# Performance work log

Measured on AMD Instinct MI355X. Metric: run time of the kernel, lower is better.

## Reference

```python
import jax, jax.numpy as jnp
import numpy as np

B, M, D = 8, 8192, 1024   # batch, tokens, latent_dim
N, P = 128, 1             # num_experts, slots_per_expert
F = 4096                  # expert_dim


def setup_inputs() -> dict:
    key = jax.random.key(0)
    k_x, k_phi, k_w1, k_b1, k_w2, k_b2 = jax.random.split(key, 6)
    x = jax.random.normal(k_x, (B, M, D), dtype=jnp.float32)
    # phi initialized as randn(d, n, p) / sqrt(d) in the original
    phi = jax.random.normal(k_phi, (D, N, P), dtype=jnp.float32) / (D ** 0.5)
    # Single shared expert MLP (original aliases one nn.Sequential across all experts)
    W1 = jax.random.normal(k_w1, (D, F), dtype=jnp.float32) / (D ** 0.5)
    b1 = jax.random.normal(k_b1, (F,), dtype=jnp.float32) * 0.01
    W2 = jax.random.normal(k_w2, (F, D), dtype=jnp.float32) / (F ** 0.5)
    b2 = jax.random.normal(k_b2, (D,), dtype=jnp.float32) * 0.01
    return {"x": x, "phi": phi, "W1": W1, "b1": b1, "W2": W2, "b2": b2}


def reference(x, phi, W1, b1, W2, b2):
    # dispatch / combine logits: [b, m, n, p]
    logits = jnp.einsum('bmd,dnp->bmnp', x, phi)
    d = jax.nn.softmax(logits, axis=1)                      # softmax over tokens m
    b_, m_, n_, p_ = logits.shape
    c = jax.nn.softmax(logits.reshape(b_, m_, n_ * p_), axis=-1).reshape(b_, m_, n_, p_)
    # slot inputs: [b, n, p, d]
    x_i = jnp.einsum('bmd,bmnp->bnpd', x, d)
    # shared expert MLP (torch GELU default = exact erf)
    h = jax.nn.gelu(jnp.einsum('bnpd,df->bnpf', x_i, W1) + b1, approximate=False)
    y_i = jnp.einsum('bnpf,fd->bnpd', h, W2) + b2
    # combine: [b, m, d]
    y = jnp.einsum('bnpd,bmnp->bmd', y_i, c)
    return y
```

## Files before the change

### kernel.cpp

```cpp
#include <hip/hip_runtime.h>
#include <math.h>

#define Bq 8
#define Mq 8192
#define Dq 1024
#define Nq 128
#define Fq 4096

typedef __bf16 bf16x8 __attribute__((ext_vector_type(8)));
typedef float f32x4 __attribute__((ext_vector_type(4)));
union P4 { __bf16 h[4]; unsigned long long u; };
union H4 { short4 v; _Float16 h[4]; };
union B8 { int4 v; __bf16 h[8]; };

__device__ __forceinline__ int swz128(int row, int bcol) {
  return row * 128 + (bcol ^ ((((row & 7) ^ ((row >> 3) & 7))) << 4));
}
__device__ __forceinline__ int swz256(int row, int bcol) {
  return row * 256 + (bcol ^ ((row & 7) << 4));
}

__global__ __launch_bounds__(256) void wconv(const float* __restrict__ src,
                                             unsigned long long* __restrict__ dst, long n4)
{
  long i = (long)blockIdx.x * 256 + threadIdx.x;
  if (i >= n4) return;
  float4 v = ((const float4*)src)[i];
  P4 p; p.h[0] = (__bf16)v.x; p.h[1] = (__bf16)v.y; p.h[2] = (__bf16)v.z; p.h[3] = (__bf16)v.w;
  dst[i] = p.u;
}

__global__ __launch_bounds__(256) void logits_mfma(
    const float* __restrict__ x, const float* __restrict__ phi,
    __bf16* __restrict__ eT, __bf16* __restrict__ cbuf)
{
  __shared__ __align__(16) char sA[16384];
  __shared__ __align__(16) char sP[16384];
  int mt = blockIdx.x, b = blockIdx.y;
  int m0 = mt * 128;
  int t = threadIdx.x;
  int col = t & 127, half = t >> 7;
  int arow = t >> 4, ac4 = t & 15;
  int w = t >> 6, l = t & 63, la = l & 15, lb = l >> 4;

  f32x4 zero = {0.f, 0.f, 0.f, 0.f};
  f32x4 acc[2][8];
  for (int i = 0; i < 2; ++i) for (int j = 0; j < 8; ++j) acc[i][j] = zero;

  for (int k0 = 0; k0 < Dq; k0 += 64) {
    #pragma unroll
    for (int i = 0; i < 8; ++i) {
      int row = arow + 16 * i;
      float4 v = *(const float4*)(x + ((long)b * Mq + m0 + row) * Dq + k0 + ac4 * 4);
      P4 p;
      p.h[0] = (__bf16)v.x; p.h[1] = (__bf16)v.y;
      p.h[2] = (__bf16)v.z; p.h[3] = (__bf16)v.w;
      *(unsigned long long*)(sA + swz128(row, 8 * ac4)) = p.u;
    }
    {
      const float* Pp = phi + (long)(k0 + half * 32) * Nq + col;
      #pragma unroll
      for (int i = 0; i < 32; i += 4) {
        float a0 = Pp[(i + 0) * Nq], a1 = Pp[(i + 1) * Nq];
        float a2 = Pp[(i + 2) * Nq], a3 = Pp[(i + 3) * Nq];
        P4 p;
        p.h[0] = (__bf16)a0; p.h[1] = (__bf16)a1;
        p.h[2] = (__bf16)a2; p.h[3] = (__bf16)a3;
        *(unsigned long long*)(sP + swz128(col, 2 * (half * 32 + i))) = p.u;
      }
    }
    __syncthreads();
    #pragma unroll
    for (int sub = 0; sub < 2; ++sub) {
      int mbyte = sub * 64 + lb * 16;
      bf16x8 af0 = *(const bf16x8*)(sA + swz128(w * 32 + la, mbyte));
      bf16x8 af1 = *(const bf16x8*)(sA + swz128(w * 32 + 16 + la, mbyte));
      bf16x8 bv[8];
      #pragma unroll
      for (int j = 0; j < 8; ++j)
        bv[j] = *(const bf16x8*)(sP + swz128(j * 16 + la, mbyte));
      #pragma unroll
      for (int j = 0; j < 8; ++j) {
        acc[0][j] = __builtin_amdgcn_mfma_f32_16x16x32_bf16(af0, bv[j], acc[0][j], 0, 0, 0);
        acc[1][j] = __builtin_amdgcn_mfma_f32_16x16x32_bf16(af1, bv[j], acc[1][j], 0, 0, 0);
      }
    }
    __syncthreads();
  }
  float inv[2][4];
  #pragma unroll
  for (int i = 0; i < 2; ++i)
    #pragma unroll
    for (int r = 0; r < 4; ++r) {
      float s = 0.f;
      #pragma unroll
      for (int j = 0; j < 8; ++j) s += __expf(acc[i][j][r]);
      s += __shfl_xor(s, 1); s += __shfl_xor(s, 2);
      s += __shfl_xor(s, 4); s += __shfl_xor(s, 8);
      inv[i][r] = 1.0f / s;
    }
  __bf16* Cb = cbuf + ((long)b * Mq + m0) * Nq;
  __bf16* Eb = eT + (long)b * Nq * Mq + m0;
  #pragma unroll
  for (int i = 0; i < 2; ++i)
    #pragma unroll
    for (int j = 0; j < 8; ++j) {
      P4 p;
      #pragma unroll
      for (int r = 0; r < 4; ++r) {
        int row = w * 32 + i * 16 + lb * 4 + r;
        float e = __expf(acc[i][j][r]);
        p.h[r] = (__bf16)e;
        Cb[(long)row * Nq + j * 16 + la] = (__bf16)(e * inv[i][r]);
      }
      *(unsigned long long*)(Eb + (long)(j * 16 + la) * Mq + w * 32 + i * 16 + lb * 4) = p.u;
    }
}

__global__ __launch_bounds__(256) void colsum_rows(const __bf16* __restrict__ eT,
                                                   float* __restrict__ cinv)
{
  __shared__ float red[4];
  int r = blockIdx.x;
  int t = threadIdx.x;
  const __bf16* p = eT + (long)r * Mq;
  float s = 0.f;
  #pragma unroll
  for (int k = 0; k < 4; ++k) {
    B8 v; v.v = *(const int4*)(p + t * 8 + k * 2048);
    #pragma unroll
    for (int e = 0; e < 8; ++e) s += (float)v.h[e];
  }
  #pragma unroll
  for (int off = 32; off >= 1; off >>= 1) s += __shfl_down(s, off);
  if ((t & 63) == 0) red[t >> 6] = s;
  __syncthreads();
  if (t == 0) cinv[r] = 1.0f / (red[0] + red[1] + red[2] + red[3]);
}

__global__ __launch_bounds__(256) void xi_mfma(
    const __bf16* __restrict__ eT, const float* __restrict__ x,
    _Float16* __restrict__ part)
{
  __shared__ __align__(16) char sD[16384];
  __shared__ __align__(16) char sX[16384];
  int lin = blockIdx.x;
  int wk = (lin & 7) * 64 + (lin >> 3);
  int dts = wk & 7, kc = (wk >> 3) & 7, b = wk >> 6;
  int d0 = dts * 128;
  int t = threadIdx.x;
  int w = t >> 6, l = t & 63, la = l & 15, lb = l >> 4;
  int arow = t >> 1, ahalf = t & 1;
  const __bf16* Ep0 = eT + ((long)b * Nq + arow) * Mq + kc * 1024 + ahalf * 32;
  int bmb = (w * 2 + (l >> 5)) * 8;
  int bd  = (l & 31) * 4;
  const float* Xp0 = x + ((long)b * Mq + kc * 1024 + bmb) * Dq + d0 + bd;

  f32x4 zero = {0.f, 0.f, 0.f, 0.f};
  f32x4 acc[2][8];
  for (int i = 0; i < 2; ++i) for (int j = 0; j < 8; ++j) acc[i][j] = zero;

  int4 ar[4];
  float br[8][4];
  #pragma unroll
  for (int q = 0; q < 4; ++q) ar[q] = *(const int4*)(Ep0 + q * 8);
  #pragma unroll
  for (int k = 0; k < 8; ++k) *(float4*)br[k] = *(const float4*)(Xp0 + (long)k * Dq);
  #pragma unroll
  for (int q = 0; q < 4; ++q) *(int4*)(sD + swz128(arow, ahalf * 64 + q * 16)) = ar[q];
  #pragma unroll
  for (int q = 0; q < 4; ++q) {
    B8 o;
    #pragma unroll
    for (int k = 0; k < 8; ++k) o.h[k] = (__bf16)br[k][q];
    *(int4*)(sX + swz128(bd + q, 2 * bmb)) = o.v;
  }

  for (int it = 0; it < 16; ++it) {
    __syncthreads();
    if (it < 15) {
      #pragma unroll
      for (int q = 0; q < 4; ++q) ar[q] = *(const int4*)(Ep0 + (it + 1) * 64 + q * 8);
      #pragma unroll
      for (int k = 0; k < 8; ++k)
        *(float4*)br[k] = *(const float4*)(Xp0 + ((long)(it + 1) * 64 + k) * Dq);
    }
    #pragma unroll
    for (int sub = 0; sub < 2; ++sub) {
      int mbyte = sub * 64 + lb * 16;
      bf16x8 af0 = *(const bf16x8*)(sD + swz128(w * 32 + la, mbyte));
      bf16x8 af1 = *(const bf16x8*)(sD + swz128(w * 32 + 16 + la, mbyte));
      #pragma unroll
      for (int j = 0; j < 8; ++j) {
        bf16x8 bv = *(const bf16x8*)(sX + swz128(j * 16 + la, mbyte));
        acc[0][j] = __builtin_amdgcn_mfma_f32_16x16x32_bf16(af0, bv, acc[0][j], 0, 0, 0);
        acc[1][j] = __builtin_amdgcn_mfma_f32_16x16x32_bf16(af1, bv, acc[1][j], 0, 0, 0);
      }
    }
    __syncthreads();
    if (it < 15) {
      #pragma unroll
      for (int q = 0; q < 4; ++q) *(int4*)(sD + swz128(arow, ahalf * 64 + q * 16)) = ar[q];
      #pragma unroll
      for (int q = 0; q < 4; ++q) {
        B8 o;
        #pragma unroll
        for (int k = 0; k < 8; ++k) o.h[k] = (__bf16)br[k][q];
        *(int4*)(sX + swz128(bd + q, 2 * bmb)) = o.v;
      }
    }
  }
  _Float16* P = part + (((long)kc * Bq + b) * 8 + dts) * 16384;
  #pragma unroll
  for (int i = 0; i < 2; ++i)
    #pragma unroll
    for (int j = 0; j < 8; ++j) {
      H4 o;
      #pragma unroll
      for (int r = 0; r < 4; ++r) o.h[r] = (_Float16)acc[i][j][r];
      *(short4*)(P + ((w * 16 + i * 8 + j) * 64 + l) * 4) = o.v;
    }
}

__global__ __launch_bounds__(256) void xi_reduce(const _Float16* __restrict__ part,
    const float* __restrict__ cinv, __bf16* __restrict__ xib)
{
  int s = blockIdx.x * 256 + threadIdx.x;
  int l = s & 63, j = (s >> 6) & 7, i = (s >> 9) & 1;
  int w = (s >> 10) & 3, dts = (s >> 12) & 7, b = s >> 15;
  const _Float16* p = part + ((long)b * 8 + dts) * 16384 + ((w * 16 + i * 8 + j) * 64 + l) * 4;
  float sum[4] = {};
  #pragma unroll
  for (int kc = 0; kc < 8; ++kc) {
    H4 v; v.v = *(const short4*)(p + (long)kc * 1048576);
    #pragma unroll
    for (int r = 0; r < 4; ++r) sum[r] += (float)v.h[r];
  }
  int lb = l >> 4, la = l & 15;
  int nbase = w * 32 + i * 16 + lb * 4;
  int d = dts * 128 + j * 16 + la;
  #pragma unroll
  for (int r = 0; r < 4; ++r) {
    int n = b * 128 + nbase + r;
    xib[(long)n * Dq + d] = (__bf16)(sum[r] * cinv[n]);
  }
}

template<int EPI, typename OT>
__global__ __launch_bounds__(256) void gemm_bf16(const __bf16* __restrict__ A,
    const __bf16* __restrict__ Bw, const float* __restrict__ bias,
    OT* __restrict__ C, int lda, int ldb, int ldc, int kLen, long strideCz)
{
  __shared__ __align__(16) char sA[16384];
  __shared__ __align__(16) char sB[16384];
  int m0 = blockIdx.x * 128, n0 = blockIdx.y * 128;
  int kbase = blockIdx.z * kLen;
  C += (long)blockIdx.z * strideCz;
  int t = threadIdx.x;
  int col = t & 127, half = t >> 7;
  int w = t >> 6, l = t & 63, la = l & 15, lb = l >> 4;

  f32x4 zero = {0.f, 0.f, 0.f, 0.f};
  f32x4 acc[2][8];
  for (int i = 0; i < 2; ++i) for (int j = 0; j < 8; ++j) acc[i][j] = zero;

  for (int kt = 0; kt < kLen; kt += 64) {
    int kp = kbase + kt;
    #pragma unroll
    for (int s = 0; s < 4; ++s) {
      int idx = t + 256 * s;
      int row = idx >> 3, c8 = idx & 7;
      *(int4*)(sA + swz128(row, c8 * 16)) =
          *(const int4*)(A + (long)(m0 + row) * lda + kp + c8 * 8);
    }
    {
      const __bf16* Bp = Bw + (long)(kp + half * 32) * ldb + n0 + col;
      #pragma unroll
      for (int i = 0; i < 32; i += 4) {
        P4 p;
        p.h[0] = Bp[(long)(i + 0) * ldb]; p.h[1] = Bp[(long)(i + 1) * ldb];
        p.h[2] = Bp[(long)(i + 2) * ldb]; p.h[3] = Bp[(long)(i + 3) * ldb];
        *(unsigned long long*)(sB + swz128(col, 2 * (half * 32 + i))) = p.u;
      }
    }
    __syncthreads();
    #pragma unroll
    for (int sub = 0; sub < 2; ++sub) {
      int mbyte = sub * 64 + lb * 16;
      bf16x8 af0 = *(const bf16x8*)(sA + swz128(w * 32 + la, mbyte));
      bf16x8 af1 = *(const bf16x8*)(sA + swz128(w * 32 + 16 + la, mbyte));
      bf16x8 bv[8];
      #pragma unroll
      for (int j = 0; j < 8; ++j)
        bv[j] = *(const bf16x8*)(sB + swz128(j * 16 + la, mbyte));
      #pragma unroll
      for (int j = 0; j < 8; ++j) {
        acc[0][j] = __builtin_amdgcn_mfma_f32_16x16x32_bf16(af0, bv[j], acc[0][j], 0, 0, 0);
        acc[1][j] = __builtin_amdgcn_mfma_f32_16x16x32_bf16(af1, bv[j], acc[1][j], 0, 0, 0);
      }
    }
    __syncthreads();
  }
  #pragma unroll
  for (int i = 0; i < 2; ++i)
    #pragma unroll
    for (int j = 0; j < 8; ++j)
      #pragma unroll
      for (int r = 0; r < 4; ++r) {
        int row = m0 + w * 32 + i * 16 + lb * 4 + r;
        int colg = n0 + j * 16 + la;
        float v = acc[i][j][r];
        if (EPI == 2) {
          v += bias[colg];
          v = 0.5f * v * (1.0f + erff(v * 0.70710678118654752f));
        }
        C[(long)row * ldc + colg] = (OT)v;
      }
}

__global__ __launch_bounds__(256) void g2_reduce(const float* __restrict__ part,
    const float* __restrict__ b2, __bf16* __restrict__ yiT)
{
  long idx = (long)blockIdx.x * 256 + threadIdx.x;
  int row = (int)(idx >> 10);
  int d = (int)(idx & 1023);
  float s = part[idx] + part[idx + 1048576] + part[idx + 2097152] + part[idx + 3145728] + b2[d];
  int b = row >> 7, n = row & 127;
  yiT[((long)b * Dq + d) * Nq + n] = (__bf16)s;
}

__global__ __launch_bounds__(256) void combine_v2(const __bf16* __restrict__ cbuf,
    const __bf16* __restrict__ yiT, float* __restrict__ y)
{
  __shared__ __align__(16) char sC[32768];
  __shared__ __align__(16) char sY[32768];
  int lin = blockIdx.x;
  int wk = (lin & 7) * 64 + (lin >> 3);
  int mt = wk & 63, b = wk >> 6;
  int m0 = mt * 128;
  int t = threadIdx.x;
  int row = t >> 1, c16b = (t & 1) * 8;
  #pragma unroll
  for (int q = 0; q < 8; ++q) {
    int c16 = c16b + q;
    *(int4*)(sC + swz256(row, c16 * 16)) =
        *(const int4*)(cbuf + ((long)b * Mq + m0 + row) * Nq + c16 * 8);
  }
  const __bf16* Yb = yiT + ((long)b * Dq + row) * Nq + c16b * 8;
  int4 yr[8];
  #pragma unroll
  for (int q = 0; q < 8; ++q) yr[q] = *(const int4*)(Yb + q * 8);

  int w = t >> 6, l = t & 63, la = l & 15, lb = l >> 4;
  f32x4 zero = {0.f, 0.f, 0.f, 0.f};

  for (int dt = 0; dt < 8; ++dt) {
    #pragma unroll
    for (int q = 0; q < 8; ++q)
      *(int4*)(sY + swz256(row, (c16b + q) * 16)) = yr[q];
    __syncthreads();
    if (dt < 7) {
      #pragma unroll
      for (int q = 0; q < 8; ++q)
        yr[q] = *(const int4*)(Yb + (long)(dt + 1) * 128 * Nq + q * 8);
    }
    f32x4 acc[2][8];
    for (int i = 0; i < 2; ++i) for (int j = 0; j < 8; ++j) acc[i][j] = zero;
    #pragma unroll
    for (int sub = 0; sub < 4; ++sub) {
      int mbyte = sub * 64 + lb * 16;
      bf16x8 af0 = *(const bf16x8*)(sC + swz256(w * 32 + la, mbyte));
      bf16x8 af1 = *(const bf16x8*)(sC + swz256(w * 32 + 16 + la, mbyte));
      #pragma unroll
      for (int j = 0; j < 8; ++j) {
        bf16x8 bv = *(const bf16x8*)(sY + swz256(j * 16 + la, mbyte));
        acc[0][j] = __builtin_amdgcn_mfma_f32_16x16x32_bf16(af0, bv, acc[0][j], 0, 0, 0);
        acc[1][j] = __builtin_amdgcn_mfma_f32_16x16x32_bf16(af1, bv, acc[1][j], 0, 0, 0);
      }
    }
    __syncthreads();
    float* Y = y + ((long)b * Mq + m0) * Dq + dt * 128;
    #pragma unroll
    for (int i = 0; i < 2; ++i)
      #pragma unroll
      for (int j = 0; j < 8; ++j)
        #pragma unroll
        for (int r = 0; r < 4; ++r)
          Y[(long)(w * 32 + i * 16 + lb * 4 + r) * Dq + j * 16 + la] = acc[i][j][r];
  }
}

extern "C" void kernel_launch(void* const* d_in, const int* in_sizes, int n_in,
                              void* d_out, int out_size, void* d_ws, size_t ws_size,
                              hipStream_t stream) {
  const float* x   = (const float*)d_in[0];
  const float* phi = (const float*)d_in[1];
  const float* W1  = (const float*)d_in[2];
  const float* b1  = (const float*)d_in[3];
  const float* W2  = (const float*)d_in[4];
  const float* b2  = (const float*)d_in[5];
  float* y = (float*)d_out;

  char* W = (char*)d_ws;
  __bf16*   cbuf   = (__bf16*)W;
  __bf16*   eT     = (__bf16*)(W + 16777216);
  __bf16*   h      = eT;
  _Float16* part   = (_Float16*)(W + 33554432);
  float*    g2part = (float*)(W + 33554432);
  __bf16*   W1b    = (__bf16*)(W + 50331648);
  __bf16*   W2b    = (__bf16*)(W + 58720256);
  __bf16*   xib    = (__bf16*)(W + 67108864);
  __bf16*   yiT    = (__bf16*)(W + 69206016);
  float*    cinv   = (float*)(W + 71303168);

  wconv<<<4096, 256, 0, stream>>>(W1, (unsigned long long*)W1b, 1048576);
  wconv<<<4096, 256, 0, stream>>>(W2, (unsigned long long*)W2b, 1048576);
  logits_mfma<<<dim3(Mq / 128, Bq), 256, 0, stream>>>(x, phi, eT, cbuf);
  colsum_rows<<<Bq * Nq, 256, 0, stream>>>(eT, cinv);
  xi_mfma<<<512, 256, 0, stream>>>(eT, x, part);
  xi_reduce<<<1024, 256, 0, stream>>>(part, cinv, xib);
  gemm_bf16<2, __bf16><<<dim3(8, 32, 1), 256, 0, stream>>>(
      xib, W1b, b1, h, Dq, Fq, Fq, 1024, 0L);
  gemm_bf16<0, float><<<dim3(8, 8, 4), 256, 0, stream>>>(
      h, W2b, nullptr, g2part, Fq, Dq, Dq, 1024, 1048576L);
  g2_reduce<<<4096, 256, 0, stream>>>(g2part, b2, yiT);
  combine_v2<<<512, 256, 0, stream>>>(cbuf, yiT, y);
}
```

Measured before the change: 404.9 us.

## Double grid sizes of logits, xi and combine kernels for more parallelism

```diff
diff --git a/kernel.cpp b/kernel.cpp
--- a/kernel.cpp
+++ b/kernel.cpp
@@ -34,28 +34,28 @@
     const float* __restrict__ x, const float* __restrict__ phi,
     __bf16* __restrict__ eT, __bf16* __restrict__ cbuf)
 {
-  __shared__ __align__(16) char sA[16384];
+  __shared__ __align__(16) char sA[8192];
   __shared__ __align__(16) char sP[16384];
   int mt = blockIdx.x, b = blockIdx.y;
-  int m0 = mt * 128;
+  int m0 = mt * 64;
   int t = threadIdx.x;
   int col = t & 127, half = t >> 7;
-  int arow = t >> 4, ac4 = t & 15;
   int w = t >> 6, l = t & 63, la = l & 15, lb = l >> 4;
 
   f32x4 zero = {0.f, 0.f, 0.f, 0.f};
-  f32x4 acc[2][8];
-  for (int i = 0; i < 2; ++i) for (int j = 0; j < 8; ++j) acc[i][j] = zero;
+  f32x4 acc[8];
+  for (int j = 0; j < 8; ++j) acc[j] = zero;
 
   for (int k0 = 0; k0 < Dq; k0 += 64) {
     #pragma unroll
-    for (int i = 0; i < 8; ++i) {
-      int row = arow + 16 * i;
-      float4 v = *(const float4*)(x + ((long)b * Mq + m0 + row) * Dq + k0 + ac4 * 4);
+    for (int s = 0; s < 4; ++s) {
+      int idx = t + 256 * s;
+      int row = idx >> 4, c4 = idx & 15;
+      float4 v = *(const float4*)(x + ((long)b * Mq + m0 + row) * Dq + k0 + c4 * 4);
       P4 p;
       p.h[0] = (__bf16)v.x; p.h[1] = (__bf16)v.y;
       p.h[2] = (__bf16)v.z; p.h[3] = (__bf16)v.w;
-      *(unsigned long long*)(sA + swz128(row, 8 * ac4)) = p.u;
+      *(unsigned long long*)(sA + swz128(row, c4 * 8)) = p.u;
     }
     {
       const float* Pp = phi + (long)(k0 + half * 32) * Nq + col;
@@ -73,48 +73,39 @@
     #pragma unroll
     for (int sub = 0; sub < 2; ++sub) {
       int mbyte = sub * 64 + lb * 16;
-      bf16x8 af0 = *(const bf16x8*)(sA + swz128(w * 32 + la, mbyte));
-      bf16x8 af1 = *(const bf16x8*)(sA + swz128(w * 32 + 16 + la, mbyte));
-      bf16x8 bv[8];
-      #pragma unroll
-      for (int j = 0; j < 8; ++j)
-        bv[j] = *(const bf16x8*)(sP + swz128(j * 16 + la, mbyte));
+      bf16x8 af = *(const bf16x8*)(sA + swz128(w * 16 + la, mbyte));
       #pragma unroll
       for (int j = 0; j < 8; ++j) {
-        acc[0][j] = __builtin_amdgcn_mfma_f32_16x16x32_bf16(af0, bv[j], acc[0][j], 0, 0, 0);
-        acc[1][j] = __builtin_amdgcn_mfma_f32_16x16x32_bf16(af1, bv[j], acc[1][j], 0, 0, 0);
-      }
-    }
-    __syncthreads();
-  }
-  float inv[2][4];
-  #pragma unroll
-  for (int i = 0; i < 2; ++i)
-    #pragma unroll
-    for (int r = 0; r < 4; ++r) {
-      float s = 0.f;
-      #pragma unroll
-      for (int j = 0; j < 8; ++j) s += __expf(acc[i][j][r]);
-      s += __shfl_xor(s, 1); s += __shfl_xor(s, 2);
-      s += __shfl_xor(s, 4); s += __shfl_xor(s, 8);
-      inv[i][r] = 1.0f / s;
-    }
+        bf16x8 bv = *(const bf16x8*)(sP + swz128(j * 16 + la, mbyte));
+        acc[j] = __builtin_amdgcn_mfma_f32_16x16x32_bf16(af, bv, acc[j], 0, 0, 0);
+      }
+    }
+    __syncthreads();
+  }
+  float inv[4];
+  #pragma unroll
+  for (int r = 0; r < 4; ++r) {
+    float s = 0.f;
+    #pragma unroll
+    for (int j = 0; j < 8; ++j) s += __expf(acc[j][r]);
+    s += __shfl_xor(s, 1); s += __shfl_xor(s, 2);
+    s += __shfl_xor(s, 4); s += __shfl_xor(s, 8);
+    inv[r] = 1.0f / s;
+  }
   __bf16* Cb = cbuf + ((long)b * Mq + m0) * Nq;
   __bf16* Eb = eT + (long)b * Nq * Mq + m0;
   #pragma unroll
-  for (int i = 0; i < 2; ++i)
-    #pragma unroll
-    for (int j = 0; j < 8; ++j) {
-      P4 p;
-      #pragma unroll
-      for (int r = 0; r < 4; ++r) {
-        int row = w * 32 + i * 16 + lb * 4 + r;
-        float e = __expf(acc[i][j][r]);
-        p.h[r] = (__bf16)e;
-        Cb[(long)row * Nq + j * 16 + la] = (__bf16)(e * inv[i][r]);
-      }
-      *(unsigned long long*)(Eb + (long)(j * 16 + la) * Mq + w * 32 + i * 16 + lb * 4) = p.u;
-    }
+  for (int j = 0; j < 8; ++j) {
+    P4 p;
+    #pragma unroll
+    for (int r = 0; r < 4; ++r) {
+      int row = w * 16 + lb * 4 + r;
+      float e = __expf(acc[j][r]);
+      p.h[r] = (__bf16)e;
+      Cb[(long)row * Nq + j * 16 + la] = (__bf16)(e * inv[r]);
+    }
+    *(unsigned long long*)(Eb + (long)(j * 16 + la) * Mq + w * 16 + lb * 4) = p.u;
+  }
 }
 
 __global__ __launch_bounds__(256) void colsum_rows(const __bf16* __restrict__ eT,
@@ -145,16 +136,16 @@
   __shared__ __align__(16) char sD[16384];
   __shared__ __align__(16) char sX[16384];
   int lin = blockIdx.x;
-  int wk = (lin & 7) * 64 + (lin >> 3);
-  int dts = wk & 7, kc = (wk >> 3) & 7, b = wk >> 6;
+  int wk = (lin & 7) * 128 + (lin >> 3);
+  int dts = wk & 7, kc = (wk >> 3) & 15, b = wk >> 7;
   int d0 = dts * 128;
   int t = threadIdx.x;
   int w = t >> 6, l = t & 63, la = l & 15, lb = l >> 4;
   int arow = t >> 1, ahalf = t & 1;
-  const __bf16* Ep0 = eT + ((long)b * Nq + arow) * Mq + kc * 1024 + ahalf * 32;
+  const __bf16* Ep0 = eT + ((long)b * Nq + arow) * Mq + kc * 512 + ahalf * 32;
   int bmb = (w * 2 + (l >> 5)) * 8;
   int bd  = (l & 31) * 4;
-  const float* Xp0 = x + ((long)b * Mq + kc * 1024 + bmb) * Dq + d0 + bd;
+  const float* Xp0 = x + ((long)b * Mq + kc * 512 + bmb) * Dq + d0 + bd;
 
   f32x4 zero = {0.f, 0.f, 0.f, 0.f};
   f32x4 acc[2][8];
@@ -176,9 +167,9 @@
     *(int4*)(sX + swz128(bd + q, 2 * bmb)) = o.v;
   }
 
-  for (int it = 0; it < 16; ++it) {
-    __syncthreads();
-    if (it < 15) {
+  for (int it = 0; it < 8; ++it) {
+    __syncthreads();
+    if (it < 7) {
       #pragma unroll
       for (int q = 0; q < 4; ++q) ar[q] = *(const int4*)(Ep0 + (it + 1) * 64 + q * 8);
       #pragma unroll
@@ -198,7 +189,7 @@
       }
     }
     __syncthreads();
-    if (it < 15) {
+    if (it < 7) {
       #pragma unroll
       for (int q = 0; q < 4; ++q) *(int4*)(sD + swz128(arow, ahalf * 64 + q * 16)) = ar[q];
       #pragma unroll
@@ -231,7 +222,7 @@
   const _Float16* p = part + ((long)b * 8 + dts) * 16384 + ((w * 16 + i * 8 + j) * 64 + l) * 4;
   float sum[4] = {};
   #pragma unroll
-  for (int kc = 0; kc < 8; ++kc) {
+  for (int kc = 0; kc < 16; ++kc) {
     H4 v; v.v = *(const short4*)(p + (long)kc * 1048576);
     #pragma unroll
     for (int r = 0; r < 4; ++r) sum[r] += (float)v.h[r];
@@ -329,37 +320,41 @@
   yiT[((long)b * Dq + d) * Nq + n] = (__bf16)s;
 }
 
-__global__ __launch_bounds__(256) void combine_v2(const __bf16* __restrict__ cbuf,
+__global__ __launch_bounds__(256) void combine_v3(const __bf16* __restrict__ cbuf,
     const __bf16* __restrict__ yiT, float* __restrict__ y)
 {
-  __shared__ __align__(16) char sC[32768];
   __shared__ __align__(16) char sY[32768];
   int lin = blockIdx.x;
-  int wk = (lin & 7) * 64 + (lin >> 3);
-  int mt = wk & 63, b = wk >> 6;
+  int wk = (lin & 7) * 128 + (lin >> 3);
+  int dtg = wk & 1, mt = (wk >> 1) & 63, b = wk >> 7;
   int m0 = mt * 128;
   int t = threadIdx.x;
+  int w = t >> 6, l = t & 63, la = l & 15, lb = l >> 4;
+
+  const __bf16* Cb = cbuf + ((long)b * Mq + m0 + w * 32 + la) * Nq + lb * 8;
+  bf16x8 af0[4], af1[4];
+  #pragma unroll
+  for (int sub = 0; sub < 4; ++sub) {
+    af0[sub] = *(const bf16x8*)(Cb + sub * 32);
+    af1[sub] = *(const bf16x8*)(Cb + 16 * Nq + sub * 32);
+  }
+
   int row = t >> 1, c16b = (t & 1) * 8;
-  #pragma unroll
-  for (int q = 0; q < 8; ++q) {
-    int c16 = c16b + q;
-    *(int4*)(sC + swz256(row, c16 * 16)) =
-        *(const int4*)(cbuf + ((long)b * Mq + m0 + row) * Nq + c16 * 8);
-  }
   const __bf16* Yb = yiT + ((long)b * Dq + row) * Nq + c16b * 8;
   int4 yr[8];
   #pragma unroll
-  for (int q = 0; q < 8; ++q) yr[q] = *(const int4*)(Yb + q * 8);
-
-  int w = t >> 6, l = t & 63, la = l & 15, lb = l >> 4;
+  for (int q = 0; q < 8; ++q)
+    yr[q] = *(const int4*)(Yb + (long)(dtg * 4) * 128 * Nq + q * 8);
+
   f32x4 zero = {0.f, 0.f, 0.f, 0.f};
-
-  for (int dt = 0; dt < 8; ++dt) {
+  for (int q4 = 0; q4 < 4; ++q4) {
+    int dt = dtg * 4 + q4;
+    __syncthreads();
     #pragma unroll
     for (int q = 0; q < 8; ++q)
       *(int4*)(sY + swz256(row, (c16b + q) * 16)) = yr[q];
     __syncthreads();
-    if (dt < 7) {
+    if (q4 < 3) {
       #pragma unroll
       for (int q = 0; q < 8; ++q)
         yr[q] = *(const int4*)(Yb + (long)(dt + 1) * 128 * Nq + q * 8);
@@ -369,16 +364,13 @@
     #pragma unroll
     for (int sub = 0; sub < 4; ++sub) {
       int mbyte = sub * 64 + lb * 16;
-      bf16x8 af0 = *(const bf16x8*)(sC + swz256(w * 32 + la, mbyte));
-      bf16x8 af1 = *(const bf16x8*)(sC + swz256(w * 32 + 16 + la, mbyte));
       #pragma unroll
       for (int j = 0; j < 8; ++j) {
         bf16x8 bv = *(const bf16x8*)(sY + swz256(j * 16 + la, mbyte));
-        acc[0][j] = __builtin_amdgcn_mfma_f32_16x16x32_bf16(af0, bv, acc[0][j], 0, 0, 0);
-        acc[1][j] = __builtin_amdgcn_mfma_f32_16x16x32_bf16(af1, bv, acc[1][j], 0, 0, 0);
-      }
-    }
-    __syncthreads();
+        acc[0][j] = __builtin_amdgcn_mfma_f32_16x16x32_bf16(af0[sub], bv, acc[0][j], 0, 0, 0);
+        acc[1][j] = __builtin_amdgcn_mfma_f32_16x16x32_bf16(af1[sub], bv, acc[1][j], 0, 0, 0);
+      }
+    }
     float* Y = y + ((long)b * Mq + m0) * Dq + dt * 128;
     #pragma unroll
     for (int i = 0; i < 2; ++i)
@@ -407,22 +399,22 @@
   __bf16*   h      = eT;
   _Float16* part   = (_Float16*)(W + 33554432);
   float*    g2part = (float*)(W + 33554432);
-  __bf16*   W1b    = (__bf16*)(W + 50331648);
-  __bf16*   W2b    = (__bf16*)(W + 58720256);
-  __bf16*   xib    = (__bf16*)(W + 67108864);
-  __bf16*   yiT    = (__bf16*)(W + 69206016);
-  float*    cinv   = (float*)(W + 71303168);
+  __bf16*   W1b    = (__bf16*)(W + 67108864);
+  __bf16*   W2b    = (__bf16*)(W + 75497472);
+  __bf16*   xib    = (__bf16*)(W + 83886080);
+  __bf16*   yiT    = (__bf16*)(W + 85983232);
+  float*    cinv   = (float*)(W + 88080384);
 
   wconv<<<4096, 256, 0, stream>>>(W1, (unsigned long long*)W1b, 1048576);
   wconv<<<4096, 256, 0, stream>>>(W2, (unsigned long long*)W2b, 1048576);
-  logits_mfma<<<dim3(Mq / 128, Bq), 256, 0, stream>>>(x, phi, eT, cbuf);
+  logits_mfma<<<dim3(Mq / 64, Bq), 256, 0, stream>>>(x, phi, eT, cbuf);
   colsum_rows<<<Bq * Nq, 256, 0, stream>>>(eT, cinv);
-  xi_mfma<<<512, 256, 0, stream>>>(eT, x, part);
+  xi_mfma<<<1024, 256, 0, stream>>>(eT, x, part);
   xi_reduce<<<1024, 256, 0, stream>>>(part, cinv, xib);
   gemm_bf16<2, __bf16><<<dim3(8, 32, 1), 256, 0, stream>>>(
       xib, W1b, b1, h, Dq, Fq, Fq, 1024, 0L);
   gemm_bf16<0, float><<<dim3(8, 8, 4), 256, 0, stream>>>(
       h, W2b, nullptr, g2part, Fq, Dq, Dq, 1024, 1048576L);
   g2_reduce<<<4096, 256, 0, stream>>>(g2part, b2, yiT);
-  combine_v2<<<512, 256, 0, stream>>>(cbuf, yiT, y);
-}
+  combine_v3<<<1024, 256, 0, stream>>>(cbuf, yiT, y);
+}
```

New measurement: 453.0 us. 1.12x slower.

## Pretranspose phi to bf16, simplify swizzles, split combine across D tiles

Applied to the files above, without the earlier changes.

```diff
diff --git a/kernel.cpp b/kernel.cpp
--- a/kernel.cpp
+++ b/kernel.cpp
@@ -14,10 +14,13 @@
 union B8 { int4 v; __bf16 h[8]; };
 
 __device__ __forceinline__ int swz128(int row, int bcol) {
-  return row * 128 + (bcol ^ ((((row & 7) ^ ((row >> 3) & 7))) << 4));
+  return row * 128 + (bcol ^ ((row & 7) << 4));
 }
 __device__ __forceinline__ int swz256(int row, int bcol) {
   return row * 256 + (bcol ^ ((row & 7) << 4));
+}
+__device__ __forceinline__ int swzX(int row, int bcol) {
+  return row * 128 + (bcol ^ ((((row & 7) ^ ((row >> 3) & 7))) << 4));
 }
 
 __global__ __launch_bounds__(256) void wconv(const float* __restrict__ src,
@@ -30,8 +33,16 @@
   dst[i] = p.u;
 }
 
+__global__ __launch_bounds__(256) void phi_conv(const float* __restrict__ src,
+                                                __bf16* __restrict__ dst)
+{
+  int idx = blockIdx.x * 256 + threadIdx.x;
+  int d = idx >> 7, n = idx & 127;
+  dst[(long)n * Dq + d] = (__bf16)src[idx];
+}
+
 __global__ __launch_bounds__(256) void logits_mfma(
-    const float* __restrict__ x, const float* __restrict__ phi,
+    const float* __restrict__ x, const __bf16* __restrict__ phiT,
     __bf16* __restrict__ eT, __bf16* __restrict__ cbuf)
 {
   __shared__ __align__(16) char sA[16384];
@@ -39,8 +50,8 @@
   int mt = blockIdx.x, b = blockIdx.y;
   int m0 = mt * 128;
   int t = threadIdx.x;
-  int col = t & 127, half = t >> 7;
   int arow = t >> 4, ac4 = t & 15;
+  int prow = t >> 1, pc = (t & 1) * 4;
   int w = t >> 6, l = t & 63, la = l & 15, lb = l >> 4;
 
   f32x4 zero = {0.f, 0.f, 0.f, 0.f};
@@ -58,16 +69,10 @@
       *(unsigned long long*)(sA + swz128(row, 8 * ac4)) = p.u;
     }
     {
-      const float* Pp = phi + (long)(k0 + half * 32) * Nq + col;
-      #pragma unroll
-      for (int i = 0; i < 32; i += 4) {
-        float a0 = Pp[(i + 0) * Nq], a1 = Pp[(i + 1) * Nq];
-        float a2 = Pp[(i + 2) * Nq], a3 = Pp[(i + 3) * Nq];
-        P4 p;
-        p.h[0] = (__bf16)a0; p.h[1] = (__bf16)a1;
-        p.h[2] = (__bf16)a2; p.h[3] = (__bf16)a3;
-        *(unsigned long long*)(sP + swz128(col, 2 * (half * 32 + i))) = p.u;
-      }
+      const __bf16* Pp = phiT + (long)prow * Dq + k0 + pc * 8;
+      #pragma unroll
+      for (int q = 0; q < 4; ++q)
+        *(int4*)(sP + swz128(prow, (pc + q) * 16)) = *(const int4*)(Pp + q * 8);
     }
     __syncthreads();
     #pragma unroll
@@ -167,13 +172,13 @@
   #pragma unroll
   for (int k = 0; k < 8; ++k) *(float4*)br[k] = *(const float4*)(Xp0 + (long)k * Dq);
   #pragma unroll
-  for (int q = 0; q < 4; ++q) *(int4*)(sD + swz128(arow, ahalf * 64 + q * 16)) = ar[q];
+  for (int q = 0; q < 4; ++q) *(int4*)(sD + swzX(arow, ahalf * 64 + q * 16)) = ar[q];
   #pragma unroll
   for (int q = 0; q < 4; ++q) {
     B8 o;
     #pragma unroll
     for (int k = 0; k < 8; ++k) o.h[k] = (__bf16)br[k][q];
-    *(int4*)(sX + swz128(bd + q, 2 * bmb)) = o.v;
+    *(int4*)(sX + swzX(bd + q, 2 * bmb)) = o.v;
   }
 
   for (int it = 0; it < 16; ++it) {
@@ -188,11 +193,11 @@
     #pragma unroll
     for (int sub = 0; sub < 2; ++sub) {
       int mbyte = sub * 64 + lb * 16;
-      bf16x8 af0 = *(const bf16x8*)(sD + swz128(w * 32 + la, mbyte));
-      bf16x8 af1 = *(const bf16x8*)(sD + swz128(w * 32 + 16 + la, mbyte));
+      bf16x8 af0 = *(const bf16x8*)(sD + swzX(w * 32 + la, mbyte));
+      bf16x8 af1 = *(const bf16x8*)(sD + swzX(w * 32 + 16 + la, mbyte));
       #pragma unroll
       for (int j = 0; j < 8; ++j) {
-        bf16x8 bv = *(const bf16x8*)(sX + swz128(j * 16 + la, mbyte));
+        bf16x8 bv = *(const bf16x8*)(sX + swzX(j * 16 + la, mbyte));
         acc[0][j] = __builtin_amdgcn_mfma_f32_16x16x32_bf16(af0, bv, acc[0][j], 0, 0, 0);
         acc[1][j] = __builtin_amdgcn_mfma_f32_16x16x32_bf16(af1, bv, acc[1][j], 0, 0, 0);
       }
@@ -200,13 +205,13 @@
     __syncthreads();
     if (it < 15) {
       #pragma unroll
-      for (int q = 0; q < 4; ++q) *(int4*)(sD + swz128(arow, ahalf * 64 + q * 16)) = ar[q];
+      for (int q = 0; q < 4; ++q) *(int4*)(sD + swzX(arow, ahalf * 64 + q * 16)) = ar[q];
       #pragma unroll
       for (int q = 0; q < 4; ++q) {
         B8 o;
         #pragma unroll
         for (int k = 0; k < 8; ++k) o.h[k] = (__bf16)br[k][q];
-        *(int4*)(sX + swz128(bd + q, 2 * bmb)) = o.v;
+        *(int4*)(sX + swzX(bd + q, 2 * bmb)) = o.v;
       }
     }
   }
@@ -329,65 +334,50 @@
   yiT[((long)b * Dq + d) * Nq + n] = (__bf16)s;
 }
 
-__global__ __launch_bounds__(256) void combine_v2(const __bf16* __restrict__ cbuf,
+__global__ __launch_bounds__(256) void combine_mfma(const __bf16* __restrict__ cbuf,
     const __bf16* __restrict__ yiT, float* __restrict__ y)
 {
   __shared__ __align__(16) char sC[32768];
   __shared__ __align__(16) char sY[32768];
   int lin = blockIdx.x;
-  int wk = (lin & 7) * 64 + (lin >> 3);
-  int mt = wk & 63, b = wk >> 6;
-  int m0 = mt * 128;
+  int wk = (lin & 7) * 512 + (lin >> 3);
+  int dt = wk & 7, mt = (wk >> 3) & 63, b = wk >> 9;
+  int m0 = mt * 128, d0 = dt * 128;
   int t = threadIdx.x;
-  int row = t >> 1, c16b = (t & 1) * 8;
-  #pragma unroll
-  for (int q = 0; q < 8; ++q) {
-    int c16 = c16b + q;
+  #pragma unroll
+  for (int s = 0; s < 8; ++s) {
+    int idx = t + 256 * s;
+    int row = idx >> 4, c16 = idx & 15;
     *(int4*)(sC + swz256(row, c16 * 16)) =
         *(const int4*)(cbuf + ((long)b * Mq + m0 + row) * Nq + c16 * 8);
-  }
-  const __bf16* Yb = yiT + ((long)b * Dq + row) * Nq + c16b * 8;
-  int4 yr[8];
-  #pragma unroll
-  for (int q = 0; q < 8; ++q) yr[q] = *(const int4*)(Yb + q * 8);
-
+    *(int4*)(sY + swz256(row, c16 * 16)) =
+        *(const int4*)(yiT + ((long)b * Dq + d0 + row) * Nq + c16 * 8);
+  }
+  __syncthreads();
   int w = t >> 6, l = t & 63, la = l & 15, lb = l >> 4;
   f32x4 zero = {0.f, 0.f, 0.f, 0.f};
-
-  for (int dt = 0; dt < 8; ++dt) {
-    #pragma unroll
-    for (int q = 0; q < 8; ++q)
-      *(int4*)(sY + swz256(row, (c16b + q) * 16)) = yr[q];
-    __syncthreads();
-    if (dt < 7) {
-      #pragma unroll
-      for (int q = 0; q < 8; ++q)
-        yr[q] = *(const int4*)(Yb + (long)(dt + 1) * 128 * Nq + q * 8);
-    }
-    f32x4 acc[2][8];
-    for (int i = 0; i < 2; ++i) for (int j = 0; j < 8; ++j) acc[i][j] = zero;
-    #pragma unroll
-    for (int sub = 0; sub < 4; ++sub) {
-      int mbyte = sub * 64 + lb * 16;
-      bf16x8 af0 = *(const bf16x8*)(sC + swz256(w * 32 + la, mbyte));
-      bf16x8 af1 = *(const bf16x8*)(sC + swz256(w * 32 + 16 + la, mbyte));
-      #pragma unroll
-      for (int j = 0; j < 8; ++j) {
-        bf16x8 bv = *(const bf16x8*)(sY + swz256(j * 16 + la, mbyte));
-        acc[0][j] = __builtin_amdgcn_mfma_f32_16x16x32_bf16(af0, bv, acc[0][j], 0, 0, 0);
-        acc[1][j] = __builtin_amdgcn_mfma_f32_16x16x32_bf16(af1, bv, acc[1][j], 0, 0, 0);
-      }
-    }
-    __syncthreads();
-    float* Y = y + ((long)b * Mq + m0) * Dq + dt * 128;
-    #pragma unroll
-    for (int i = 0; i < 2; ++i)
-      #pragma unroll
-      for (int j = 0; j < 8; ++j)
-        #pragma unroll
-        for (int r = 0; r < 4; ++r)
-          Y[(long)(w * 32 + i * 16 + lb * 4 + r) * Dq + j * 16 + la] = acc[i][j][r];
-  }
+  f32x4 acc[2][8];
+  for (int i = 0; i < 2; ++i) for (int j = 0; j < 8; ++j) acc[i][j] = zero;
+  #pragma unroll
+  for (int sub = 0; sub < 4; ++sub) {
+    int mbyte = sub * 64 + lb * 16;
+    bf16x8 af0 = *(const bf16x8*)(sC + swz256(w * 32 + la, mbyte));
+    bf16x8 af1 = *(const bf16x8*)(sC + swz256(w * 32 + 16 + la, mbyte));
+    #pragma unroll
+    for (int j = 0; j < 8; ++j) {
+      bf16x8 bv = *(const bf16x8*)(sY + swz256(j * 16 + la, mbyte));
+      acc[0][j] = __builtin_amdgcn_mfma_f32_16x16x32_bf16(af0, bv, acc[0][j], 0, 0, 0);
+      acc[1][j] = __builtin_amdgcn_mfma_f32_16x16x32_bf16(af1, bv, acc[1][j], 0, 0, 0);
+    }
+  }
+  float* Y = y + ((long)b * Mq + m0) * Dq + d0;
+  #pragma unroll
+  for (int i = 0; i < 2; ++i)
+    #pragma unroll
+    for (int j = 0; j < 8; ++j)
+      #pragma unroll
+      for (int r = 0; r < 4; ++r)
+        Y[(long)(w * 32 + i * 16 + lb * 4 + r) * Dq + j * 16 + la] = acc[i][j][r];
 }
 
 extern "C" void kernel_launch(void* const* d_in, const int* in_sizes, int n_in,
@@ -412,10 +402,12 @@
   __bf16*   xib    = (__bf16*)(W + 67108864);
   __bf16*   yiT    = (__bf16*)(W + 69206016);
   float*    cinv   = (float*)(W + 71303168);
+  __bf16*   phiT   = (__bf16*)(W + 75497472);
 
   wconv<<<4096, 256, 0, stream>>>(W1, (unsigned long long*)W1b, 1048576);
   wconv<<<4096, 256, 0, stream>>>(W2, (unsigned long long*)W2b, 1048576);
-  logits_mfma<<<dim3(Mq / 128, Bq), 256, 0, stream>>>(x, phi, eT, cbuf);
+  phi_conv<<<512, 256, 0, stream>>>(phi, phiT);
+  logits_mfma<<<dim3(Mq / 128, Bq), 256, 0, stream>>>(x, phiT, eT, cbuf);
   colsum_rows<<<Bq * Nq, 256, 0, stream>>>(eT, cinv);
   xi_mfma<<<512, 256, 0, stream>>>(eT, x, part);
   xi_reduce<<<1024, 256, 0, stream>>>(part, cinv, xib);
@@ -424,5 +416,5 @@
   gemm_bf16<0, float><<<dim3(8, 8, 4), 256, 0, stream>>>(
       h, W2b, nullptr, g2part, Fq, Dq, Dq, 1024, 1048576L);
   g2_reduce<<<4096, 256, 0, stream>>>(g2part, b2, yiT);
-  combine_v2<<<512, 256, 0, stream>>>(cbuf, yiT, y);
-}
+  combine_mfma<<<4096, 256, 0, stream>>>(cbuf, yiT, y);
+}
```

New measurement: 365.1 us. 9.8% less time.
